# Kernel optimization log

Hardware: AMD Instinct MI355X
Metric: run time of the kernel (lower is better)

Reference implementation:

```python
import jax, jax.numpy as jnp
import numpy as np

EPS = 1e-6
NUM_GROUPS = 32


def group_norm(x, w, b):
    # x: [B, C, W, H, L]
    B, C = x.shape[0], x.shape[1]
    xr = x.reshape(B, NUM_GROUPS, C // NUM_GROUPS, -1)
    mu = jnp.mean(xr, axis=(2, 3), keepdims=True)
    var = jnp.var(xr, axis=(2, 3), keepdims=True)
    xn = ((xr - mu) * jax.lax.rsqrt(var + EPS)).reshape(x.shape)
    return xn * w[None, :, None, None, None] + b[None, :, None, None, None]


def setup_inputs() -> dict:
    key = jax.random.key(0)
    ks = jax.random.split(key, 8)
    B, C, W, H, L = 2, 512, 16, 16, 16
    s = 1.0 / np.sqrt(C)
    return {
        "x": jax.random.normal(ks[0], (B, C, W, H, L), dtype=jnp.float32),
        "gn_w": jnp.ones((C,), dtype=jnp.float32),
        "gn_b": jnp.zeros((C,), dtype=jnp.float32),
        "q_w": jax.random.normal(ks[1], (C, C), dtype=jnp.float32) * s,
        "q_b": jnp.zeros((C,), dtype=jnp.float32),
        "k_w": jax.random.normal(ks[2], (C, C), dtype=jnp.float32) * s,
        "k_b": jnp.zeros((C,), dtype=jnp.float32),
        "v_w": jax.random.normal(ks[3], (C, C), dtype=jnp.float32) * s,
        "v_b": jnp.zeros((C,), dtype=jnp.float32),
        "p_w": jax.random.normal(ks[4], (C, C), dtype=jnp.float32) * s,
        "p_b": jnp.zeros((C,), dtype=jnp.float32),
    }


def reference(x, gn_w, gn_b, q_w, q_b, k_w, k_b, v_w, v_b, p_w, p_b):
    B, C, W, H, L = x.shape
    h = group_norm(x, gn_w, gn_b)
    hf = h.reshape(B, C, -1)  # [B, C, N]
    # 1x1 Conv3d == channel matmul: out[b,o,n] = sum_c w[o,c] * h[b,c,n] + b[o]
    q = jnp.einsum('oc,bcn->bon', q_w, hf) + q_b[None, :, None]
    k = jnp.einsum('oc,bcn->bon', k_w, hf) + k_b[None, :, None]
    v = jnp.einsum('oc,bcn->bon', v_w, hf) + v_b[None, :, None]
    scale = jnp.asarray(C, x.dtype) ** -0.5
    # w_[b,i,j] = sum_c q[b,c,i] * k[b,c,j]
    w_ = jnp.einsum('bci,bcj->bij', q, k) * scale
    w_ = jax.nn.softmax(w_, axis=2)
    # h_[b,c,i] = sum_j v[b,c,j] * w_[b,i,j]
    attn = jnp.einsum('bcj,bij->bci', v, w_)
    proj = jnp.einsum('oc,bcn->bon', p_w, attn) + p_b[None, :, None]
    return x + proj.reshape(B, C, W, H, L)
```

## Files before the change

### kernel.cpp

```cpp
#include <hip/hip_runtime.h>
#include <type_traits>


typedef __bf16 bf16;
typedef __attribute__((ext_vector_type(8))) __bf16 bf16x8;
typedef __attribute__((ext_vector_type(4))) __bf16 bf16x4;
typedef __attribute__((ext_vector_type(4))) float f32x4;

#define CC 512
#define NN 4096
#define BM 128
#define BN 128
#define BK 64
#define SCALE_L2E 0.06376237870903338f

__device__ __forceinline__ void gload16(const bf16* g, bf16* l) {
    __builtin_amdgcn_global_load_lds(
        (const __attribute__((address_space(1))) unsigned int*)g,
        (__attribute__((address_space(3))) unsigned int*)l, 16, 0, 0);
}

__device__ __forceinline__ void gemm_core(
    const bf16* __restrict__ A, int lda,
    const bf16* __restrict__ B, int ldb,
    int kBeg, int kEnd, int m0, int n0, f32x4 acc[4][4])
{
    __shared__ __align__(16) bf16 Als[2][BM][BK];
    __shared__ __align__(16) bf16 Bls[2][BN][BK];
    const int t    = threadIdx.x;
    const int lane = t & 63;
    const int wid  = t >> 6;
    const int wm   = (wid >> 1) * 64;
    const int wn   = (wid & 1) * 64;
    const int fr   = lane & 15;
    const int kq   = lane >> 4;
    const int r_   = t >> 3;
    const int cbs  = (t & 7) ^ (r_ & 7);
    const int dcol = (t & 7) * 8;
    const int cs0  = ((kq)     ^ (fr & 7)) * 8;
    const int cs1  = ((kq + 4) ^ (fr & 7)) * 8;

    const bf16* Ab = A + (size_t)(m0 + r_) * lda + cbs * 8;
    const bf16* Bb = B + (size_t)(n0 + r_) * ldb + cbs * 8;

#define STAGE_G(bufi, kk) do {                                              \
        _Pragma("unroll")                                                   \
        for (int i = 0; i < 4; ++i)                                         \
            gload16(Ab + (kk) + (size_t)(i * 32) * lda,                     \
                    &Als[bufi][i * 32 + r_][dcol]);                         \
        _Pragma("unroll")                                                   \
        for (int i = 0; i < 4; ++i)                                         \
            gload16(Bb + (kk) + (size_t)(i * 32) * ldb,                     \
                    &Bls[bufi][i * 32 + r_][dcol]);                         \
    } while (0)

    int cur = 0;
    STAGE_G(0, kBeg);
    __syncthreads();
    for (int k0 = kBeg; k0 < kEnd; k0 += BK) {
        if (k0 + BK < kEnd) STAGE_G(cur ^ 1, k0 + BK);
        #pragma unroll
        for (int h = 0; h < 2; ++h) {
            const int cs = h ? cs1 : cs0;
            bf16x8 af[4], bg[4];
            #pragma unroll
            for (int f = 0; f < 4; ++f) {
                af[f] = *(const bf16x8*)&Als[cur][wm + f * 16 + fr][cs];
                bg[f] = *(const bf16x8*)&Bls[cur][wn + f * 16 + fr][cs];
            }
            #pragma unroll
            for (int fm = 0; fm < 4; ++fm)
                #pragma unroll
                for (int fn = 0; fn < 4; ++fn)
                    acc[fm][fn] = __builtin_amdgcn_mfma_f32_16x16x32_bf16(
                        af[fm], bg[fn], acc[fm][fn], 0, 0, 0);
        }
        __syncthreads();
        cur ^= 1;
    }
#undef STAGE_G
}

__device__ __forceinline__ void gemm_core64(
    const bf16* __restrict__ A, int lda,
    const bf16* __restrict__ B, int ldb,
    int kBeg, int kEnd, int m0, int n0, f32x4 acc[2][4])
{
    __shared__ __align__(16) bf16 Als[2][64][BK];
    __shared__ __align__(16) bf16 Bls[2][BN][BK];
    const int t    = threadIdx.x;
    const int lane = t & 63;
    const int wid  = t >> 6;
    const int wm   = (wid >> 1) * 32;
    const int wn   = (wid & 1) * 64;
    const int fr   = lane & 15;
    const int kq   = lane >> 4;
    const int r_   = t >> 3;
    const int cbs  = (t & 7) ^ (r_ & 7);
    const int dcol = (t & 7) * 8;
    const int cs0  = ((kq)     ^ (fr & 7)) * 8;
    const int cs1  = ((kq + 4) ^ (fr & 7)) * 8;

    const bf16* Ab = A + (size_t)(m0 + r_) * lda + cbs * 8;
    const bf16* Bb = B + (size_t)(n0 + r_) * ldb + cbs * 8;

#define STAGE_G64(bufi, kk) do {                                            \
        _Pragma("unroll")                                                   \
        for (int i = 0; i < 2; ++i)                                         \
            gload16(Ab + (kk) + (size_t)(i * 32) * lda,                     \
                    &Als[bufi][i * 32 + r_][dcol]);                         \
        _Pragma("unroll")                                                   \
        for (int i = 0; i < 4; ++i)                                         \
            gload16(Bb + (kk) + (size_t)(i * 32) * ldb,                     \
                    &Bls[bufi][i * 32 + r_][dcol]);                         \
    } while (0)

    int cur = 0;
    STAGE_G64(0, kBeg);
    __syncthreads();
    for (int k0 = kBeg; k0 < kEnd; k0 += BK) {
        if (k0 + BK < kEnd) STAGE_G64(cur ^ 1, k0 + BK);
        #pragma unroll
        for (int h = 0; h < 2; ++h) {
            const int cs = h ? cs1 : cs0;
            bf16x8 af[2], bg[4];
            #pragma unroll
            for (int f = 0; f < 2; ++f)
                af[f] = *(const bf16x8*)&Als[cur][wm + f * 16 + fr][cs];
            #pragma unroll
            for (int f = 0; f < 4; ++f)
                bg[f] = *(const bf16x8*)&Bls[cur][wn + f * 16 + fr][cs];
            #pragma unroll
            for (int fm = 0; fm < 2; ++fm)
                #pragma unroll
                for (int fn = 0; fn < 4; ++fn)
                    acc[fm][fn] = __builtin_amdgcn_mfma_f32_16x16x32_bf16(
                        af[fm], bg[fn], acc[fm][fn], 0, 0, 0);
        }
        __syncthreads();
        cur ^= 1;
    }
#undef STAGE_G64
}

__global__ __launch_bounds__(256) void convert_w_kernel(
    const float* __restrict__ qw, const float* __restrict__ kw,
    const float* __restrict__ pw, bf16* __restrict__ dst)
{
    const int which = blockIdx.y;
    const float* src = which == 0 ? qw : which == 1 ? kw : pw;
    const int slot  = which == 2 ? 3 : which;
    bf16* d = dst + (size_t)slot * (CC * CC);
    const int f4 = blockIdx.x * 256 + threadIdx.x;
    float4 v = ((const float4*)src)[f4];
    bf16x4 o;
    o[0] = (bf16)v.x; o[1] = (bf16)v.y; o[2] = (bf16)v.z; o[3] = (bf16)v.w;
    ((bf16x4*)d)[f4] = o;
}

__global__ __launch_bounds__(256) void vwT_kernel(
    const float* __restrict__ vw, bf16* __restrict__ vwT)
{
    const int k0 = blockIdx.x * 64;
    const int c0 = blockIdx.y * 64;
    const int t  = threadIdx.x;
    const int tk = t & 15, tc = t >> 4;
    float o[4][4];
    #pragma unroll
    for (int j = 0; j < 4; ++j) {
        const int c = c0 + tc * 4 + j;
        float4 v = *(const float4*)(vw + (size_t)c * CC + k0 + tk * 4);
        o[j][0] = v.x; o[j][1] = v.y; o[j][2] = v.z; o[j][3] = v.w;
    }
    #pragma unroll
    for (int i = 0; i < 4; ++i) {
        bf16x4 w4;
        w4[0] = (bf16)o[0][i]; w4[1] = (bf16)o[1][i];
        w4[2] = (bf16)o[2][i]; w4[3] = (bf16)o[3][i];
        *(bf16x4*)(vwT + (size_t)(k0 + tk * 4 + i) * CC + c0 + tc * 4) = w4;
    }
}

__global__ __launch_bounds__(256) void wb_kernel(
    const float* __restrict__ pw, const float* __restrict__ vb,
    float* __restrict__ wb)
{
    const int o = blockIdx.x * 256 + threadIdx.x;
    const float4* row = (const float4*)(pw + (size_t)o * CC);
    const float4* v4  = (const float4*)vb;
    float s = 0.f;
    #pragma unroll 4
    for (int i = 0; i < 128; ++i) {
        float4 a = row[i], b = v4[i];
        s += a.x * b.x + a.y * b.y + a.z * b.z + a.w * b.w;
    }
    wb[o] = s;
}

__global__ __launch_bounds__(256) void gn_stats_kernel(
    const float* __restrict__ x, float* __restrict__ mr)
{
    const int bg = blockIdx.x >> 2;
    const int qq = blockIdx.x & 3;
    const float4* base = (const float4*)(x + (size_t)bg * 16 * NN);
    const int t = threadIdx.x;
    float s = 0.f, sq = 0.f;
    #pragma unroll 4
    for (int i = 0; i < 16; ++i) {
        float4 v = base[(qq * 16 + i) * 256 + t];
        s  += v.x + v.y + v.z + v.w;
        sq += v.x * v.x + v.y * v.y + v.z * v.z + v.w * v.w;
    }
    #pragma unroll
    for (int o = 32; o > 0; o >>= 1) { s += __shfl_xor(s, o); sq += __shfl_xor(sq, o); }
    __shared__ float rs[4], rq[4];
    const int lane = t & 63, wid = t >> 6;
    if (lane == 0) { rs[wid] = s; rq[wid] = sq; }
    __syncthreads();
    if (t == 0) {
        atomicAdd(&mr[bg * 2],     rs[0] + rs[1] + rs[2] + rs[3]);
        atomicAdd(&mr[bg * 2 + 1], rq[0] + rq[1] + rq[2] + rq[3]);
    }
}

__global__ __launch_bounds__(256) void gn_apply_T_kernel(
    const float* __restrict__ x, const float* __restrict__ gw,
    const float* __restrict__ gb, const float* __restrict__ mr,
    bf16* __restrict__ hT)
{
    const int b  = blockIdx.z;
    const int n0 = blockIdx.x * 64;
    const int c0 = blockIdx.y * 64;
    const int t  = threadIdx.x;
    const int tn = t & 15, tc = t >> 4;
    float o[4][4];
    #pragma unroll
    for (int j = 0; j < 4; ++j) {
        const int c = c0 + tc * 4 + j;
        const int bg = b * 32 + (c >> 4);
        const float invn = 1.f / 65536.f;
        const float mean = mr[bg * 2] * invn;
        const float var  = mr[bg * 2 + 1] * invn - mean * mean;
        const float rstd = rsqrtf(var + 1e-6f);
        const float w  = gw[c] * rstd;
        const float bb = gb[c] - mean * w;
        float4 v = *(const float4*)(x + ((size_t)(b * CC + c)) * NN + n0 + tn * 4);
        o[j][0] = v.x * w + bb; o[j][1] = v.y * w + bb;
        o[j][2] = v.z * w + bb; o[j][3] = v.w * w + bb;
    }
    bf16* dst = hT + (size_t)b * (size_t)NN * CC;
    #pragma unroll
    for (int i = 0; i < 4; ++i) {
        bf16x4 w4;
        w4[0] = (bf16)o[0][i]; w4[1] = (bf16)o[1][i];
        w4[2] = (bf16)o[2][i]; w4[3] = (bf16)o[3][i];
        *(bf16x4*)(dst + (size_t)(n0 + tn * 4 + i) * CC + c0 + tc * 4) = w4;
    }
}

__global__ __launch_bounds__(256) void fw_gemm_kernel(
    const bf16* __restrict__ pwb, const bf16* __restrict__ vwT,
    bf16* __restrict__ fw)
{
    const int m0 = blockIdx.y * BM, n0 = blockIdx.x * BN;
    f32x4 acc[4][4] = {};
    gemm_core(pwb, CC, vwT, CC, 0, CC, m0, n0, acc);
    const int lane = threadIdx.x & 63, wid = threadIdx.x >> 6;
    const int wm = (wid >> 1) * 64, wn = (wid & 1) * 64;
    const int cf = lane & 15, rb = (lane >> 4) * 4;
    #pragma unroll
    for (int fm = 0; fm < 4; ++fm)
      #pragma unroll
      for (int fn = 0; fn < 4; ++fn)
        #pragma unroll
        for (int r = 0; r < 4; ++r)
            fw[(size_t)(m0 + wm + fm * 16 + rb + r) * CC
               + (n0 + wn + fn * 16 + cf)] = (bf16)acc[fm][fn][r];
}

__global__ __launch_bounds__(256) void qkw_gemm_kernel(
    const bf16* __restrict__ hT, const bf16* __restrict__ wbf,
    const bf16* __restrict__ fw,
    const float* __restrict__ qb, const float* __restrict__ kb,
    bf16* __restrict__ qT, bf16* __restrict__ kT, bf16* __restrict__ Wt)
{
    const size_t CN = (size_t)CC * NN;
    const int id = blockIdx.x;
    const int seg = id >> 7, s = id & 127;

    const bf16* A; const bf16* B;
    int m0, n0, ldo; bf16* outp; const float* bias; int role;
    if (seg < 4) {
        role = seg & 1;
        const int b = seg >> 1;
        A = hT + (size_t)b * CN;
        B = wbf + (size_t)role * CC * CC;
        m0 = (s >> 2) * 128; n0 = (s & 3) * 128;
        outp = (role ? kT : qT) + (size_t)b * CN; ldo = CC;
        bias = role ? kb : qb;
    } else {
        role = 2;
        const int b = seg - 4;
        A = fw;
        B = hT + (size_t)b * CN;
        m0 = (s >> 5) * 128; n0 = (s & 31) * 128;
        outp = Wt + (size_t)b * CN; ldo = NN;
        bias = nullptr;
    }
    f32x4 acc[4][4] = {};
    gemm_core(A, CC, B, CC, 0, CC, m0, n0, acc);
    const int lane = threadIdx.x & 63, wid = threadIdx.x >> 6;
    const int wm = (wid >> 1) * 64, wn = (wid & 1) * 64;
    const int cf = lane & 15, rb = (lane >> 4) * 4;
    #pragma unroll
    for (int fm = 0; fm < 4; ++fm)
      #pragma unroll
      for (int fn = 0; fn < 4; ++fn) {
          const int col = n0 + wn + fn * 16 + cf;
          const float bv = (role < 2) ? bias[col] : 0.f;
          #pragma unroll
          for (int r = 0; r < 4; ++r) {
              const int row = m0 + wm + fm * 16 + rb + r;
              float val = acc[fm][fn][r] + bv;
              if (role == 0) val *= SCALE_L2E;
              outp[(size_t)row * ldo + col] = (bf16)val;
          }
      }
}

__global__ __launch_bounds__(512) void se8_kernel(
    const bf16* __restrict__ qT, const bf16* __restrict__ kT,
    bf16* __restrict__ E, float* __restrict__ rowsum)
{
    __shared__ __align__(16) bf16 Als[2][256][64];
    __shared__ __align__(16) bf16 Bls[2][256][64];

    const int b = blockIdx.z;
    const size_t CN = (size_t)CC * NN;
    const bf16* A = qT + (size_t)b * CN;
    const bf16* Bm = kT + (size_t)b * CN;
    const int m0 = blockIdx.y * 256, n0 = blockIdx.x * 256;

    const int t    = threadIdx.x;
    const int lane = t & 63;
    const int wid  = t >> 6;
    const int wr   = wid >> 2;
    const int wc   = wid & 3;
    const int fr   = lane & 15;
    const int kq   = lane >> 4;
    const int cs0  = ((kq)     ^ (fr & 7)) * 8;
    const int cs1  = ((kq + 4) ^ (fr & 7)) * 8;

    const int rr0 = t >> 3;
    const int bl0 = t & 7;

    auto SB = [&](int kt, int h) {
        #pragma unroll
        for (int j = 0; j < 2; ++j) {
            const int r = rr0 + j * 64 + h * 128;
            const int src = bl0 ^ (r & 7);
            gload16(Bm + (size_t)(n0 + r) * CC + kt * 64 + src * 8,
                    &Bls[kt & 1][r][bl0 * 8]);
        }
    };
    auto SA = [&](int kt, int s) {
        #pragma unroll
        for (int j = 0; j < 2; ++j) {
            const int r = rr0 + s * 64 + j * 128;
            const int src = bl0 ^ (r & 7);
            gload16(A + (size_t)(m0 + r) * CC + kt * 64 + src * 8,
                    &Als[kt & 1][r][bl0 * 8]);
        }
    };

    f32x4 acc[8][4] = {};
    bf16x8 bf_[4][2];

    auto phase = [&](int kt, auto qc, auto stage, int waitmode) {
        constexpr int Q = decltype(qc)::value;
        const int db = kt & 1;
        if (Q == 0) {
            #pragma unroll
            for (int g = 0; g < 4; ++g) {
                const int br = wc * 64 + g * 16 + fr;
                bf_[g][0] = *(const bf16x8*)&Bls[db][br][cs0];
                bf_[g][1] = *(const bf16x8*)&Bls[db][br][cs1];
            }
        }
        bf16x8 af_[2][2];
        #pragma unroll
        for (int f = 0; f < 2; ++f) {
            const int ar = wr * 128 + Q * 32 + f * 16 + fr;
            af_[f][0] = *(const bf16x8*)&Als[db][ar][cs0];
            af_[f][1] = *(const bf16x8*)&Als[db][ar][cs1];
        }
        stage();
        if (waitmode == 1)      asm volatile("s_waitcnt vmcnt(6)" ::: "memory");
        else if (waitmode == 2) asm volatile("s_waitcnt vmcnt(0)" ::: "memory");
        __builtin_amdgcn_s_barrier();
        asm volatile("s_waitcnt lgkmcnt(0)" ::: "memory");
        __builtin_amdgcn_sched_barrier(0);
        __builtin_amdgcn_s_setprio(1);
        #pragma unroll
        for (int kh = 0; kh < 2; ++kh)
            #pragma unroll
            for (int f = 0; f < 2; ++f)
                #pragma unroll
                for (int g = 0; g < 4; ++g)
                    acc[Q * 2 + f][g] = __builtin_amdgcn_mfma_f32_16x16x32_bf16(
                        af_[f][kh], bf_[g][kh], acc[Q * 2 + f][g], 0, 0, 0);
        __builtin_amdgcn_s_setprio(0);
        __builtin_amdgcn_s_barrier();
    };

    SB(0, 0); SB(0, 1); SA(0, 0); SA(0, 1);
    SB(1, 0); SB(1, 1); SA(1, 0);
    asm volatile("s_waitcnt vmcnt(6)" ::: "memory");
    __builtin_amdgcn_s_barrier();

    #define IC(v) std::integral_constant<int, v>{}
    for (int i = 0; i < 4; ++i) {
        const int k0t = 2 * i, k1t = 2 * i + 1;
        const int T2 = 2 * i + 2, T3 = 2 * i + 3;
        const bool more = (i < 3);
        const int wm_ = more ? 1 : 2;
        phase(k0t, IC(0), [&]{ SA(k1t, 1); },            0);
        phase(k0t, IC(1), [&]{ if (more) SB(T2, 0); },   0);
        phase(k0t, IC(2), [&]{ if (more) SB(T2, 1); },   0);
        phase(k0t, IC(3), [&]{ if (more) SA(T2, 0); },   wm_);
        phase(k1t, IC(0), [&]{ if (more) SA(T2, 1); },   0);
        phase(k1t, IC(1), [&]{ if (more) SB(T3, 0); },   0);
        phase(k1t, IC(2), [&]{ if (more) SB(T3, 1); },   0);
        phase(k1t, IC(3), [&]{ if (more) SA(T3, 0); },   wm_);
    }
    #undef IC

    bf16* E_b = E + (size_t)b * NN * NN;
    float* rs_b = rowsum + (size_t)b * NN;
    const int cf = fr, rb = kq * 4;
    #pragma unroll
    for (int fm = 0; fm < 8; ++fm)
      #pragma unroll
      for (int g = 0; g < 4; ++g)
        #pragma unroll
        for (int r = 0; r < 4; ++r) {
            float e = exp2f(fminf(acc[fm][g][r], 86.f));
            acc[fm][g][r] = e;
            E_b[(size_t)(m0 + wr * 128 + fm * 16 + rb + r) * NN
                + (n0 + wc * 64 + g * 16 + cf)] = (bf16)e;
        }
    #pragma unroll
    for (int fm = 0; fm < 8; ++fm)
      #pragma unroll
      for (int r = 0; r < 4; ++r) {
          float s = acc[fm][0][r] + acc[fm][1][r] + acc[fm][2][r] + acc[fm][3][r];
          s += __shfl_xor(s, 1); s += __shfl_xor(s, 2);
          s += __shfl_xor(s, 4); s += __shfl_xor(s, 8);
          if (cf == 0)
              atomicAdd(&rs_b[m0 + wr * 128 + fm * 16 + rb + r], s);
      }
}

__global__ __launch_bounds__(256) void pvproj_kernel(
    const bf16* __restrict__ Wt, const bf16* __restrict__ E,
    const float* __restrict__ rowsum, const float* __restrict__ wb,
    const float* __restrict__ pb, const float* __restrict__ x,
    float* __restrict__ outp)
{
    const int b = blockIdx.z;
    const size_t CN = (size_t)CC * NN;
    const int m0 = blockIdx.y * 64, n0 = blockIdx.x * BN;
    f32x4 acc[2][4] = {};
    gemm_core64(Wt + (size_t)b * CN, NN, E + (size_t)b * NN * NN, NN,
                0, NN, m0, n0, acc);
    const float* rs_b = rowsum + (size_t)b * NN;
    const int lane = threadIdx.x & 63, wid = threadIdx.x >> 6;
    const int wm = (wid >> 1) * 32, wn = (wid & 1) * 64;
    const int cf = lane & 15, rb = (lane >> 4) * 4;
    #pragma unroll
    for (int fm = 0; fm < 2; ++fm)
      #pragma unroll
      for (int g = 0; g < 4; ++g) {
          const int col = n0 + wn + g * 16 + cf;
          const float inv = 1.f / rs_b[col];
          #pragma unroll
          for (int r = 0; r < 4; ++r) {
              const int row = m0 + wm + fm * 16 + rb + r;
              const size_t idx = (size_t)b * CN + (size_t)row * NN + col;
              outp[idx] = acc[fm][g][r] * inv + wb[row] + pb[row] + x[idx];
          }
      }
}

extern "C" void kernel_launch(void* const* d_in, const int* in_sizes, int n_in,
                              void* d_out, int out_size, void* d_ws, size_t ws_size,
                              hipStream_t stream)
{
    const float* x   = (const float*)d_in[0];
    const float* gnw = (const float*)d_in[1];
    const float* gnb = (const float*)d_in[2];
    const float* qw  = (const float*)d_in[3];
    const float* qb  = (const float*)d_in[4];
    const float* kw  = (const float*)d_in[5];
    const float* kb  = (const float*)d_in[6];
    const float* vw  = (const float*)d_in[7];
    const float* vb  = (const float*)d_in[8];
    const float* pw  = (const float*)d_in[9];
    const float* pb  = (const float*)d_in[10];
    float* outp = (float*)d_out;

    char* ws = (char*)d_ws;
    size_t off = 0;
    auto alloc = [&](size_t bytes) -> char* {
        char* p = ws + off;
        off = (off + bytes + 255) & ~(size_t)255;
        return p;
    };
    const size_t CN = (size_t)CC * NN;
    bf16*  wbf  = (bf16*)alloc(4 * (size_t)CC * CC * sizeof(bf16));
    bf16*  hT   = (bf16*)alloc(2 * CN * sizeof(bf16));
    bf16*  qT   = (bf16*)alloc(2 * CN * sizeof(bf16));
    bf16*  kT   = (bf16*)alloc(2 * CN * sizeof(bf16));
    bf16*  fw   = (bf16*)alloc((size_t)CC * CC * sizeof(bf16));
    bf16*  Wt   = (bf16*)alloc(2 * CN * sizeof(bf16));
    bf16*  E    = (bf16*)alloc(2 * (size_t)NN * NN * sizeof(bf16));
    float* rowsum = (float*)alloc(2 * NN * sizeof(float));
    float* wb   = (float*)alloc(CC * sizeof(float));
    float* mr   = (float*)alloc(64 * 2 * sizeof(float));

    bf16* vwT = wbf + 2 * (size_t)CC * CC;
    bf16* pwb = wbf + 3 * (size_t)CC * CC;

    convert_w_kernel<<<dim3(256, 3), 256, 0, stream>>>(qw, kw, pw, wbf);
    vwT_kernel<<<dim3(8, 8), 256, 0, stream>>>(vw, vwT);
    wb_kernel<<<2, 256, 0, stream>>>(pw, vb, wb);
    hipMemsetAsync(mr, 0, 64 * 2 * sizeof(float), stream);
    gn_stats_kernel<<<256, 256, 0, stream>>>(x, mr);
    gn_apply_T_kernel<<<dim3(NN / 64, CC / 64, 2), 256, 0, stream>>>(
        x, gnw, gnb, mr, hT);
    hipMemsetAsync(rowsum, 0, 2 * NN * sizeof(float), stream);

    fw_gemm_kernel<<<dim3(4, 4), 256, 0, stream>>>(pwb, vwT, fw);
    qkw_gemm_kernel<<<768, 256, 0, stream>>>(
        hT, wbf, fw, qb, kb, qT, kT, Wt);

    se8_kernel<<<dim3(16, 16, 2), 512, 0, stream>>>(qT, kT, E, rowsum);

    pvproj_kernel<<<dim3(NN / BN, 8, 2), 256, 0, stream>>>(
        Wt, E, rowsum, wb, pb, x, outp);
}
```

Before: 202.2 us.

## Fold K projection into Q via precomputed Wk^T Wq, dropping K GEMM

```diff
diff --git a/kernel.cpp b/kernel.cpp
--- a/kernel.cpp
+++ b/kernel.cpp
@@ -143,24 +143,23 @@
 #undef STAGE_G64
 }
 
-__global__ __launch_bounds__(256) void convert_w_kernel(
-    const float* __restrict__ qw, const float* __restrict__ kw,
+__global__ __launch_bounds__(256) void convert_pw_kernel(
     const float* __restrict__ pw, bf16* __restrict__ dst)
 {
-    const int which = blockIdx.y;
-    const float* src = which == 0 ? qw : which == 1 ? kw : pw;
-    const int slot  = which == 2 ? 3 : which;
-    bf16* d = dst + (size_t)slot * (CC * CC);
     const int f4 = blockIdx.x * 256 + threadIdx.x;
-    float4 v = ((const float4*)src)[f4];
+    float4 v = ((const float4*)pw)[f4];
     bf16x4 o;
     o[0] = (bf16)v.x; o[1] = (bf16)v.y; o[2] = (bf16)v.z; o[3] = (bf16)v.w;
-    ((bf16x4*)d)[f4] = o;
-}
-
-__global__ __launch_bounds__(256) void vwT_kernel(
-    const float* __restrict__ vw, bf16* __restrict__ vwT)
-{
+    ((bf16x4*)dst)[f4] = o;
+}
+
+__global__ __launch_bounds__(256) void transposeT_kernel(
+    const float* __restrict__ qw, const float* __restrict__ kw,
+    const float* __restrict__ vw, bf16* __restrict__ wbf)
+{
+    const int z = blockIdx.z;
+    const float* src = z == 0 ? qw : z == 1 ? kw : vw;
+    bf16* dst = wbf + (size_t)z * CC * CC;
     const int k0 = blockIdx.x * 64;
     const int c0 = blockIdx.y * 64;
     const int t  = threadIdx.x;
@@ -169,7 +168,7 @@
     #pragma unroll
     for (int j = 0; j < 4; ++j) {
         const int c = c0 + tc * 4 + j;
-        float4 v = *(const float4*)(vw + (size_t)c * CC + k0 + tk * 4);
+        float4 v = *(const float4*)(src + (size_t)c * CC + k0 + tk * 4);
         o[j][0] = v.x; o[j][1] = v.y; o[j][2] = v.z; o[j][3] = v.w;
     }
     #pragma unroll
@@ -177,7 +176,7 @@
         bf16x4 w4;
         w4[0] = (bf16)o[0][i]; w4[1] = (bf16)o[1][i];
         w4[2] = (bf16)o[2][i]; w4[3] = (bf16)o[3][i];
-        *(bf16x4*)(vwT + (size_t)(k0 + tk * 4 + i) * CC + c0 + tc * 4) = w4;
+        *(bf16x4*)(dst + (size_t)(k0 + tk * 4 + i) * CC + c0 + tc * 4) = w4;
     }
 }
 
@@ -195,6 +194,45 @@
         s += a.x * b.x + a.y * b.y + a.z * b.z + a.w * b.w;
     }
     wb[o] = s;
+}
+
+__global__ __launch_bounds__(256) void u_kernel(
+    const bf16* __restrict__ kwT, const float* __restrict__ qb,
+    float* __restrict__ u)
+{
+    const int d = blockIdx.x * 256 + threadIdx.x;
+    const bf16x8* row = (const bf16x8*)(kwT + (size_t)d * CC);
+    float s = 0.f;
+    for (int i = 0; i < 64; ++i) {
+        bf16x8 v = row[i];
+        #pragma unroll
+        for (int j = 0; j < 8; ++j) s += (float)v[j] * qb[i * 8 + j];
+    }
+    u[d] = s;
+}
+
+__global__ __launch_bounds__(256) void cvec_kernel(
+    const float* __restrict__ u, const bf16* __restrict__ hT,
+    const float* __restrict__ qb, const float* __restrict__ kb,
+    float* __restrict__ cvec)
+{
+    const int j = blockIdx.x * 256 + threadIdx.x;
+    const bf16x8* row = (const bf16x8*)(hT + (size_t)j * CC);
+    float s = 0.f;
+    for (int i = 0; i < 64; ++i) {
+        bf16x8 v = row[i];
+        #pragma unroll
+        for (int t8 = 0; t8 < 8; ++t8) s += (float)v[t8] * u[i * 8 + t8];
+    }
+    float qk = 0.f;
+    const float4* q4 = (const float4*)qb;
+    const float4* k4 = (const float4*)kb;
+    #pragma unroll 4
+    for (int i = 0; i < 128; ++i) {
+        float4 a = q4[i], b = k4[i];
+        qk += a.x * b.x + a.y * b.y + a.z * b.z + a.w * b.w;
+    }
+    cvec[j] = SCALE_L2E * (s + qk);
 }
 
 __global__ __launch_bounds__(256) void gn_stats_kernel(
@@ -258,55 +296,14 @@
     }
 }
 
-__global__ __launch_bounds__(256) void fw_gemm_kernel(
-    const bf16* __restrict__ pwb, const bf16* __restrict__ vwT,
-    bf16* __restrict__ fw)
-{
+__global__ __launch_bounds__(256) void fwMb_kernel(
+    const bf16* __restrict__ wbf, bf16* __restrict__ fw, bf16* __restrict__ Mb)
+{
+    const int z = blockIdx.z;
+    const bf16* A = z == 0 ? wbf + 3 * (size_t)CC * CC : wbf + 1 * (size_t)CC * CC;
+    const bf16* B = z == 0 ? wbf + 2 * (size_t)CC * CC : wbf + 0 * (size_t)CC * CC;
+    bf16* outp = z == 0 ? fw : Mb;
     const int m0 = blockIdx.y * BM, n0 = blockIdx.x * BN;
-    f32x4 acc[4][4] = {};
-    gemm_core(pwb, CC, vwT, CC, 0, CC, m0, n0, acc);
-    const int lane = threadIdx.x & 63, wid = threadIdx.x >> 6;
-    const int wm = (wid >> 1) * 64, wn = (wid & 1) * 64;
-    const int cf = lane & 15, rb = (lane >> 4) * 4;
-    #pragma unroll
-    for (int fm = 0; fm < 4; ++fm)
-      #pragma unroll
-      for (int fn = 0; fn < 4; ++fn)
-        #pragma unroll
-        for (int r = 0; r < 4; ++r)
-            fw[(size_t)(m0 + wm + fm * 16 + rb + r) * CC
-               + (n0 + wn + fn * 16 + cf)] = (bf16)acc[fm][fn][r];
-}
-
-__global__ __launch_bounds__(256) void qkw_gemm_kernel(
-    const bf16* __restrict__ hT, const bf16* __restrict__ wbf,
-    const bf16* __restrict__ fw,
-    const float* __restrict__ qb, const float* __restrict__ kb,
-    bf16* __restrict__ qT, bf16* __restrict__ kT, bf16* __restrict__ Wt)
-{
-    const size_t CN = (size_t)CC * NN;
-    const int id = blockIdx.x;
-    const int seg = id >> 7, s = id & 127;
-
-    const bf16* A; const bf16* B;
-    int m0, n0, ldo; bf16* outp; const float* bias; int role;
-    if (seg < 4) {
-        role = seg & 1;
-        const int b = seg >> 1;
-        A = hT + (size_t)b * CN;
-        B = wbf + (size_t)role * CC * CC;
-        m0 = (s >> 2) * 128; n0 = (s & 3) * 128;
-        outp = (role ? kT : qT) + (size_t)b * CN; ldo = CC;
-        bias = role ? kb : qb;
-    } else {
-        role = 2;
-        const int b = seg - 4;
-        A = fw;
-        B = hT + (size_t)b * CN;
-        m0 = (s >> 5) * 128; n0 = (s & 31) * 128;
-        outp = Wt + (size_t)b * CN; ldo = NN;
-        bias = nullptr;
-    }
     f32x4 acc[4][4] = {};
     gemm_core(A, CC, B, CC, 0, CC, m0, n0, acc);
     const int lane = threadIdx.x & 63, wid = threadIdx.x >> 6;
@@ -315,21 +312,58 @@
     #pragma unroll
     for (int fm = 0; fm < 4; ++fm)
       #pragma unroll
+      for (int fn = 0; fn < 4; ++fn)
+        #pragma unroll
+        for (int r = 0; r < 4; ++r)
+            outp[(size_t)(m0 + wm + fm * 16 + rb + r) * CC
+                 + (n0 + wn + fn * 16 + cf)] = (bf16)acc[fm][fn][r];
+}
+
+__global__ __launch_bounds__(256) void qkw_gemm_kernel(
+    const bf16* __restrict__ hT, const bf16* __restrict__ Mb,
+    const bf16* __restrict__ fw,
+    bf16* __restrict__ qT, bf16* __restrict__ Wt)
+{
+    const size_t CN = (size_t)CC * NN;
+    const int id = blockIdx.x;
+    const int seg = id >> 7, s = id & 127;
+
+    const bf16* A; const bf16* B;
+    int m0, n0, ldo; bf16* outp; bool scale;
+    if (seg < 2) {
+        const int b = seg;
+        A = hT + (size_t)b * CN;  B = Mb;
+        m0 = (s >> 2) * 128; n0 = (s & 3) * 128;
+        outp = qT + (size_t)b * CN; ldo = CC; scale = true;
+    } else {
+        const int b = seg - 2;
+        A = fw;  B = hT + (size_t)b * CN;
+        m0 = (s >> 5) * 128; n0 = (s & 31) * 128;
+        outp = Wt + (size_t)b * CN; ldo = NN; scale = false;
+    }
+    f32x4 acc[4][4] = {};
+    gemm_core(A, CC, B, CC, 0, CC, m0, n0, acc);
+    const int lane = threadIdx.x & 63, wid = threadIdx.x >> 6;
+    const int wm = (wid >> 1) * 64, wn = (wid & 1) * 64;
+    const int cf = lane & 15, rb = (lane >> 4) * 4;
+    #pragma unroll
+    for (int fm = 0; fm < 4; ++fm)
+      #pragma unroll
       for (int fn = 0; fn < 4; ++fn) {
           const int col = n0 + wn + fn * 16 + cf;
-          const float bv = (role < 2) ? bias[col] : 0.f;
           #pragma unroll
           for (int r = 0; r < 4; ++r) {
               const int row = m0 + wm + fm * 16 + rb + r;
-              float val = acc[fm][fn][r] + bv;
-              if (role == 0) val *= SCALE_L2E;
+              float val = acc[fm][fn][r];
+              if (scale) val *= SCALE_L2E;
               outp[(size_t)row * ldo + col] = (bf16)val;
           }
       }
 }
 
 __global__ __launch_bounds__(512) void se8_kernel(
-    const bf16* __restrict__ qT, const bf16* __restrict__ kT,
+    const bf16* __restrict__ qT, const bf16* __restrict__ hTg,
+    const float* __restrict__ cvec,
     bf16* __restrict__ E, float* __restrict__ rowsum)
 {
     __shared__ __align__(16) bf16 Als[2][256][64];
@@ -337,8 +371,8 @@
 
     const int b = blockIdx.z;
     const size_t CN = (size_t)CC * NN;
-    const bf16* A = qT + (size_t)b * CN;
-    const bf16* Bm = kT + (size_t)b * CN;
+    const bf16* A  = qT + (size_t)b * CN;
+    const bf16* Bm = hTg + (size_t)b * CN;
     const int m0 = blockIdx.y * 256, n0 = blockIdx.x * 256;
 
     const int t    = threadIdx.x;
@@ -437,14 +471,19 @@
 
     bf16* E_b = E + (size_t)b * NN * NN;
     float* rs_b = rowsum + (size_t)b * NN;
+    const float* cv = cvec + (size_t)b * NN;
     const int cf = fr, rb = kq * 4;
+    float cvv[4];
+    #pragma unroll
+    for (int g = 0; g < 4; ++g)
+        cvv[g] = cv[n0 + wc * 64 + g * 16 + cf];
     #pragma unroll
     for (int fm = 0; fm < 8; ++fm)
       #pragma unroll
       for (int g = 0; g < 4; ++g)
         #pragma unroll
         for (int r = 0; r < 4; ++r) {
-            float e = exp2f(fminf(acc[fm][g][r], 86.f));
+            float e = exp2f(fminf(acc[fm][g][r] + cvv[g], 86.f));
             acc[fm][g][r] = e;
             E_b[(size_t)(m0 + wr * 128 + fm * 16 + rb + r) * NN
                 + (n0 + wc * 64 + g * 16 + cf)] = (bf16)e;
@@ -520,31 +559,34 @@
     bf16*  wbf  = (bf16*)alloc(4 * (size_t)CC * CC * sizeof(bf16));
     bf16*  hT   = (bf16*)alloc(2 * CN * sizeof(bf16));
     bf16*  qT   = (bf16*)alloc(2 * CN * sizeof(bf16));
-    bf16*  kT   = (bf16*)alloc(2 * CN * sizeof(bf16));
     bf16*  fw   = (bf16*)alloc((size_t)CC * CC * sizeof(bf16));
+    bf16*  Mb   = (bf16*)alloc((size_t)CC * CC * sizeof(bf16));
     bf16*  Wt   = (bf16*)alloc(2 * CN * sizeof(bf16));
     bf16*  E    = (bf16*)alloc(2 * (size_t)NN * NN * sizeof(bf16));
     float* rowsum = (float*)alloc(2 * NN * sizeof(float));
+    float* cvec = (float*)alloc(2 * NN * sizeof(float));
+    float* u    = (float*)alloc(CC * sizeof(float));
     float* wb   = (float*)alloc(CC * sizeof(float));
     float* mr   = (float*)alloc(64 * 2 * sizeof(float));
 
-    bf16* vwT = wbf + 2 * (size_t)CC * CC;
+    bf16* kwT = wbf + 1 * (size_t)CC * CC;
     bf16* pwb = wbf + 3 * (size_t)CC * CC;
 
-    convert_w_kernel<<<dim3(256, 3), 256, 0, stream>>>(qw, kw, pw, wbf);
-    vwT_kernel<<<dim3(8, 8), 256, 0, stream>>>(vw, vwT);
+    convert_pw_kernel<<<256, 256, 0, stream>>>(pw, pwb);
+    transposeT_kernel<<<dim3(8, 8, 3), 256, 0, stream>>>(qw, kw, vw, wbf);
     wb_kernel<<<2, 256, 0, stream>>>(pw, vb, wb);
     hipMemsetAsync(mr, 0, 64 * 2 * sizeof(float), stream);
     gn_stats_kernel<<<256, 256, 0, stream>>>(x, mr);
     gn_apply_T_kernel<<<dim3(NN / 64, CC / 64, 2), 256, 0, stream>>>(
         x, gnw, gnb, mr, hT);
+    u_kernel<<<2, 256, 0, stream>>>(kwT, qb, u);
+    cvec_kernel<<<32, 256, 0, stream>>>(u, hT, qb, kb, cvec);
     hipMemsetAsync(rowsum, 0, 2 * NN * sizeof(float), stream);
 
-    fw_gemm_kernel<<<dim3(4, 4), 256, 0, stream>>>(pwb, vwT, fw);
-    qkw_gemm_kernel<<<768, 256, 0, stream>>>(
-        hT, wbf, fw, qb, kb, qT, kT, Wt);
-
-    se8_kernel<<<dim3(16, 16, 2), 512, 0, stream>>>(qT, kT, E, rowsum);
+    fwMb_kernel<<<dim3(4, 4, 2), 256, 0, stream>>>(wbf, fw, Mb);
+    qkw_gemm_kernel<<<512, 256, 0, stream>>>(hT, Mb, fw, qT, Wt);
+
+    se8_kernel<<<dim3(16, 16, 2), 512, 0, stream>>>(qT, hT, cvec, E, rowsum);
 
     pvproj_kernel<<<dim3(NN / BN, 8, 2), 256, 0, stream>>>(
         Wt, E, rowsum, wb, pb, x, outp);
```

Measured after the change: 225.6 us. 11.6% more time.
